# Kernel optimization log

Hardware: AMD Instinct MI355X
Metric: run time of the kernel (lower is better)

## Reference

```python
import jax, jax.numpy as jnp
import numpy as np

B_, S_, D_ = 2, 1024, 768
EXPAND, HEADDIM, DSTATE = 2, 64, 64
DINNER = EXPAND * D_            # 1536
NHEADS = DINNER // HEADDIM      # 24
DMLP = int(2.5 * D_)            # 1920
PROJ = 2 * DINNER + 2 * NHEADS * DSTATE + NHEADS + NHEADS * (DSTATE // 2)  # 6936


def rms_norm(x, w, eps=1e-5):
    return x * jax.lax.rsqrt(jnp.mean(x * x, axis=-1, keepdims=True) + eps) * w


def apply_rope(x, angles):
    # x: (..., d_state), angles: (..., d_state//2)
    x1 = x[..., 0::2]
    x2 = x[..., 1::2]
    c, s = jnp.cos(angles), jnp.sin(angles)
    even = c * x1 - s * x2
    odd = s * x1 + c * x2
    return jnp.stack([even, odd], axis=-1).reshape(x.shape)


def ssm_scan(x, A, Bm, Cm):
    # x: (b,s,h,p), A: (b,s,h), Bm/Cm: (b,s,h,n)
    b, s, h, p = x.shape
    n = Bm.shape[-1]

    def step(hstate, inp):
        x_t, A_t, B_t, C_t = inp
        hstate = hstate * jnp.exp(A_t)[:, :, None, None] + jnp.einsum('bhn,bhp->bhpn', B_t, x_t)
        y_t = jnp.einsum('bhpn,bhn->bhp', hstate, C_t)
        return hstate, y_t

    h0 = jnp.zeros((b, h, p, n), dtype=x.dtype)
    xs = (jnp.swapaxes(x, 0, 1), jnp.swapaxes(A, 0, 1),
          jnp.swapaxes(Bm, 0, 1), jnp.swapaxes(Cm, 0, 1))
    _, ys = jax.lax.scan(step, h0, xs)
    return jnp.swapaxes(ys, 0, 1)  # (b,s,h,p)


def setup_inputs() -> dict:
    key = jax.random.key(0)
    ks = jax.random.split(key, 16)
    sc = 0.02
    return {
        'x': jax.random.normal(ks[0], (B_, S_, D_), dtype=jnp.float32),
        'norm1_w': jnp.ones((D_,), jnp.float32),
        'norm2_w': jnp.ones((D_,), jnp.float32),
        'in_proj_w': jax.random.normal(ks[1], (PROJ, D_), jnp.float32) * sc,
        'out_proj_w': jax.random.normal(ks[2], (D_, DINNER), jnp.float32) * sc,
        'A_log': jax.random.uniform(ks[3], (NHEADS,), jnp.float32, -4.0, -1.0),
        'D': jnp.ones((NHEADS,), jnp.float32),
        'dt_bias': jax.random.uniform(ks[4], (NHEADS,), jnp.float32, 0.001, 0.1),
        'B_bias': jnp.ones((1, NHEADS, DSTATE), jnp.float32),
        'C_bias': jnp.ones((1, NHEADS, DSTATE), jnp.float32),
        'Bnorm_w': jnp.ones((DSTATE,), jnp.float32),
        'Cnorm_w': jnp.ones((DSTATE,), jnp.float32),
        'mlp_gate_w': jax.random.normal(ks[5], (DMLP, D_), jnp.float32) * sc,
        'mlp_up_w': jax.random.normal(ks[6], (DMLP, D_), jnp.float32) * sc,
        'mlp_down_w': jax.random.normal(ks[7], (D_, DMLP), jnp.float32) * sc,
    }


def reference(x, norm1_w, norm2_w, in_proj_w, out_proj_w, A_log, D, dt_bias,
              B_bias, C_bias, Bnorm_w, Cnorm_w, mlp_gate_w, mlp_up_w, mlp_down_w):
    b, s, _ = x.shape
    h = rms_norm(x, norm1_w)
    proj = jnp.einsum('bsd,od->bso', h, in_proj_w)
    i = 0
    z = proj[..., i:i + DINNER]; i += DINNER
    x_ssm = proj[..., i:i + DINNER]; i += DINNER
    Bm = proj[..., i:i + NHEADS * DSTATE].reshape(b, s, NHEADS, DSTATE); i += NHEADS * DSTATE
    Cm = proj[..., i:i + NHEADS * DSTATE].reshape(b, s, NHEADS, DSTATE); i += NHEADS * DSTATE
    dt = proj[..., i:i + NHEADS]; i += NHEADS
    theta = proj[..., i:].reshape(b, s, NHEADS, DSTATE // 2)

    dt = jax.nn.softplus(dt + dt_bias)                 # (b,s,h)
    A = -jnp.exp(A_log) * dt                           # (b,s,h)
    alpha = jnp.exp(A)
    gamma = (alpha - 1.0) / (A + 1e-6) * 0.5 + 1.0

    Bm = rms_norm(Bm, Bnorm_w) + B_bias
    Cm = rms_norm(Cm, Cnorm_w) + C_bias
    cum_theta = jnp.cumsum(dt[..., None] * theta, axis=1)
    Bm = apply_rope(Bm, cum_theta)
    Cm = apply_rope(Cm, cum_theta)

    x_ssm = x_ssm.reshape(b, s, NHEADS, HEADDIM)
    x_scaled = x_ssm * gamma[..., None]
    y = ssm_scan(x_scaled, A, Bm, Cm)                  # (b,s,h,p)
    skip = (D[None, None, :] * x_ssm.sum(-1))[..., None]  # (b,s,h,1)
    y = (y + skip).reshape(b, s, DINNER)
    y = y * (z * jax.nn.sigmoid(z))
    y = jnp.einsum('bsi,oi->bso', y, out_proj_w)
    x = x + y
    h2 = rms_norm(x, norm2_w)
    g = jnp.einsum('bsd,od->bso', h2, mlp_gate_w)
    u = jnp.einsum('bsd,od->bso', h2, mlp_up_w)
    mlp = jnp.einsum('bsi,oi->bso', (g * jax.nn.sigmoid(g)) * u, mlp_down_w)
    return x + mlp
```

## Files before the change

kernel.cpp:

```cpp
#include <hip/hip_runtime.h>

typedef unsigned short u16;
typedef __attribute__((ext_vector_type(8))) short short8;
typedef __attribute__((ext_vector_type(4))) float f32x4;

constexpr int B_N    = 2;
constexpr int SEQ    = 1024;
constexpr int DMODEL = 768;
constexpr int DINNER = 1536;
constexpr int NH     = 24;
constexpr int DMLP   = 1920;
constexpr int NPROJ  = 6936;
constexpr int PP     = 7040;
constexpr int MROWS  = B_N * SEQ;
constexpr int NCHUNK = 16;
constexpr int CLEN   = 64;

__device__ __forceinline__ u16 f2bf(float f) {
  union { float f; unsigned u; } x; x.f = f;
  unsigned r = x.u + 0x7fffu + ((x.u >> 16) & 1u);
  return (u16)(r >> 16);
}

__device__ __forceinline__ void gld_lds16(const u16* g, u16* l) {
  __builtin_amdgcn_global_load_lds((const __attribute__((address_space(1))) void*)g,
                                   (__attribute__((address_space(3))) void*)l, 16, 0, 0);
}

__device__ __forceinline__ short8 frag(const u16* base, int row, int cb) {
  return *(const short8*)(base + row * 64 + ((cb ^ (row & 7)) << 3));
}
__device__ __forceinline__ int swz_idx(int row, int e) {
  return (((e >> 3) ^ (row & 7)) << 3) | (e & 7);
}

constexpr size_t E0  = (size_t)PP * DMODEL;
constexpr size_t E0s = (size_t)NPROJ * DMODEL;
constexpr size_t E1  = (size_t)DMODEL * DINNER;
constexpr size_t E2  = (size_t)DMLP * DMODEL;
constexpr size_t ETOT = E0 + E1 + 3 * E2;

__global__ void cast_all_kernel(const float* __restrict__ w_in, const float* __restrict__ w_out,
                                const float* __restrict__ w_g, const float* __restrict__ w_u,
                                const float* __restrict__ w_d,
                                u16* __restrict__ wb_in, u16* __restrict__ wb_out,
                                u16* __restrict__ wb_gu, u16* __restrict__ wb_d) {
  size_t i = ((size_t)blockIdx.x * 256 + threadIdx.x) * 4;
  if (i >= ETOT) return;
  float4 v; u16* dst;
  if (i < E0) {
    dst = wb_in + i;
    if (i < E0s) v = *(const float4*)(w_in + i);
    else { v.x = v.y = v.z = v.w = 0.f; }
  } else if (i < E0 + E1) {
    size_t k = i - E0; dst = wb_out + k; v = *(const float4*)(w_out + k);
  } else if (i < E0 + E1 + E2) {
    size_t k = i - E0 - E1; dst = wb_gu + k; v = *(const float4*)(w_g + k);
  } else if (i < E0 + E1 + 2 * E2) {
    size_t k = i - E0 - E1 - E2; dst = wb_gu + E2 + k; v = *(const float4*)(w_u + k);
  } else {
    size_t k = i - E0 - E1 - 2 * E2; dst = wb_d + k; v = *(const float4*)(w_d + k);
  }
  short4 o;
  o.x = (short)f2bf(v.x); o.y = (short)f2bf(v.y);
  o.z = (short)f2bf(v.z); o.w = (short)f2bf(v.w);
  *(short4*)dst = o;
}

__global__ __launch_bounds__(256) void add_rmsnorm_kernel(
    const float* __restrict__ a, const float* __restrict__ b,
    const float* __restrict__ w, float* __restrict__ sum_out,
    u16* __restrict__ hout) {
  int row = blockIdx.x;
  int t = threadIdx.x;
  const float* pa = a + (size_t)row * DMODEL;
  const float* pb = b ? b + (size_t)row * DMODEL : nullptr;
  float v[3]; float ss = 0.f;
#pragma unroll
  for (int i = 0; i < 3; ++i) {
    int c = t + i * 256;
    float x = pa[c];
    if (pb) x += pb[c];
    v[i] = x; ss += x * x;
  }
#pragma unroll
  for (int o = 32; o > 0; o >>= 1) ss += __shfl_xor(ss, o);
  __shared__ float red[4];
  if ((t & 63) == 0) red[t >> 6] = ss;
  __syncthreads();
  ss = red[0] + red[1] + red[2] + red[3];
  float sc = rsqrtf(ss * (1.f / DMODEL) + 1e-5f);
#pragma unroll
  for (int i = 0; i < 3; ++i) {
    int c = t + i * 256;
    if (sum_out) sum_out[(size_t)row * DMODEL + c] = v[i];
    hout[(size_t)row * DMODEL + c] = f2bf(v[i] * sc * w[c]);
  }
}

template<int BM>
__global__ __launch_bounds__(256) void gemm_bt_kernel(
    const u16* __restrict__ A, const u16* __restrict__ Bw,
    float* __restrict__ C, int K, int ldc, const float* __restrict__ addsrc) {
  constexpr int MI = BM / 32;
  __shared__ u16 As[BM * 64];
  __shared__ u16 Bs[128 * 64];
  const int t = threadIdx.x;
  const int lane = t & 63;
  const int wave = t >> 6;
  const int wm = wave >> 1, wn = wave & 1;
  const int gx = gridDim.x, gy = gridDim.y;
  const int o = blockIdx.y * gx + blockIdx.x;
  const int nwg = gx * gy;
  const int cid = (o & 7) * (nwg >> 3) + (o >> 3);
  const int bx = cid / gy, by = cid - bx * gy;
  const int m0 = by * BM, n0 = bx * 128;
  f32x4 acc[MI][4] = {};
  const int rr = t >> 3;
  const int kc = (t & 7) * 8;
  const u16* ga = A + (size_t)(m0 + rr) * K + kc;
  const u16* gb = Bw + (size_t)(n0 + rr) * K + kc;
  for (int kt = 0; kt < K; kt += 64) {
    __syncthreads();
#pragma unroll
    for (int i = 0; i < MI; ++i)
      gld_lds16(ga + (size_t)i * 32 * K + kt, As + i * 2048 + t * 8);
#pragma unroll
    for (int i = 0; i < 4; ++i)
      gld_lds16(gb + (size_t)i * 32 * K + kt, Bs + i * 2048 + t * 8);
    __syncthreads();
#pragma unroll
    for (int kh = 0; kh < 2; ++kh) {
      short8 af[MI], bfr[4];
#pragma unroll
      for (int i = 0; i < MI; ++i)
        af[i] = *(const short8*)(As + (wm * (BM / 2) + i * 16 + (lane & 15)) * 64 + kh * 32 + (lane >> 4) * 8);
#pragma unroll
      for (int j = 0; j < 4; ++j)
        bfr[j] = *(const short8*)(Bs + (wn * 64 + j * 16 + (lane & 15)) * 64 + kh * 32 + (lane >> 4) * 8);
#pragma unroll
      for (int i = 0; i < MI; ++i)
#pragma unroll
        for (int j = 0; j < 4; ++j)
          acc[i][j] = __builtin_amdgcn_mfma_f32_16x16x32_bf16(af[i], bfr[j], acc[i][j], 0, 0, 0);
    }
  }
  const int cr = (lane >> 4) * 4;
  const int cc = lane & 15;
#pragma unroll
  for (int i = 0; i < MI; ++i) {
#pragma unroll
    for (int j = 0; j < 4; ++j) {
      int row = m0 + wm * (BM / 2) + i * 16 + cr;
      int col = n0 + wn * 64 + j * 16 + cc;
      float* cp = C + (size_t)row * ldc + col;
      if (addsrc) {
        const float* ap = addsrc + (size_t)row * ldc + col;
#pragma unroll
        for (int r = 0; r < 4; ++r) cp[(size_t)r * ldc] = acc[i][j][r] + ap[(size_t)r * ldc];
      } else {
#pragma unroll
        for (int r = 0; r < 4; ++r) cp[(size_t)r * ldc] = acc[i][j][r];
      }
    }
  }
}

__global__ __launch_bounds__(256) void prep_kernel(
    float* __restrict__ proj, const float* __restrict__ A_log,
    const float* __restrict__ Dv, const float* __restrict__ dt_bias,
    const float* __restrict__ B_bias, const float* __restrict__ C_bias,
    const float* __restrict__ Bnw, const float* __restrict__ Cnw,
    float* __restrict__ Abuf, float* __restrict__ skip_b,
    float* __restrict__ dtheta) {
  int wid = blockIdx.x * 4 + (threadIdx.x >> 6);
  int lane = threadIdx.x & 63;
  int m = wid / NH, h = wid - m * NH;
  float* row = proj + (size_t)m * PP;

  float Braw = row[3072 + h * 64 + lane];
  float Craw = row[4608 + h * 64 + lane];
  float sb = Braw * Braw, sc2 = Craw * Craw;
#pragma unroll
  for (int o = 32; o > 0; o >>= 1) { sb += __shfl_xor(sb, o); sc2 += __shfl_xor(sc2, o); }
  float rb = rsqrtf(sb * (1.f / 64.f) + 1e-5f);
  float rc = rsqrtf(sc2 * (1.f / 64.f) + 1e-5f);
  row[3072 + h * 64 + lane] = Braw * rb * Bnw[lane] + B_bias[h * 64 + lane];
  row[4608 + h * 64 + lane] = Craw * rc * Cnw[lane] + C_bias[h * 64 + lane];

  float dtr = row[6144 + h] + dt_bias[h];
  float dt = dtr > 20.f ? dtr : log1pf(expf(dtr));
  float A = -expf(A_log[h]) * dt;
  float alpha = expf(A);
  float gamma = (alpha - 1.f) / (A + 1e-6f) * 0.5f + 1.f;

  float xv = row[1536 + h * 64 + lane];
  float sx = xv;
#pragma unroll
  for (int o = 32; o > 0; o >>= 1) sx += __shfl_xor(sx, o);
  row[1536 + h * 64 + lane] = xv * gamma;

  if (lane == 0) {
    Abuf[(size_t)m * NH + h] = A;
    skip_b[(size_t)m * NH + h] = Dv[h] * sx;
  }
  if (lane < 32) {
    float th = row[6168 + h * 32 + lane];
    dtheta[(size_t)m * 768 + h * 32 + lane] = dt * th;
  }
}

__global__ __launch_bounds__(256) void cumsum_a_kernel(float* __restrict__ dtheta,
                                                       float* __restrict__ ctot) {
  int bid = blockIdx.x;
  int cb = bid % 3, rest = bid / 3;
  int c = rest & 15, b = rest >> 4;
  int col = cb * 256 + threadIdx.x;
  float* p = dtheta + ((size_t)(b * SEQ + c * CLEN)) * 768 + col;
  float acc = 0.f;
#pragma unroll 4
  for (int s = 0; s < CLEN; ++s) {
    acc += p[(size_t)s * 768];
    p[(size_t)s * 768] = acc;
  }
  ctot[((size_t)b * NCHUNK + c) * 768 + col] = acc;
}

__global__ void cumsum_b_kernel(float* __restrict__ ctot) {
  int tid = blockIdx.x * 256 + threadIdx.x;
  int b = tid / 768, col = tid - b * 768;
  float pre = 0.f;
#pragma unroll
  for (int c = 0; c < NCHUNK; ++c) {
    size_t o = ((size_t)b * NCHUNK + c) * 768 + col;
    float v = ctot[o];
    ctot[o] = pre;
    pre += v;
  }
}

__global__ __launch_bounds__(256) void houtA_kernel(
    const float* __restrict__ proj, const float* __restrict__ Abuf,
    const float* __restrict__ dtheta, const float* __restrict__ ctot,
    float* __restrict__ Lbuf, float* __restrict__ Hbuf) {
  int c = blockIdx.x & 15, bh = blockIdx.x >> 4;
  int b = bh / NH, h = bh - b * NH;
  int t = threadIdx.x, w = t >> 6, l = t & 63;
  __shared__ float sTmp[64][65];
  __shared__ u16 sBT[64 * 64];
  __shared__ u16 sXT[64 * 64];
  __shared__ float sRatio[64];
  int m0 = b * SEQ + c * CLEN;
  if (w == 0) {
    float v = Abuf[(size_t)(m0 + l) * NH + h];
#pragma unroll
    for (int o = 1; o < 64; o <<= 1) {
      float u = __shfl_up(v, o);
      if (l >= o) v += u;
    }
    Lbuf[(size_t)(m0 + l) * NH + h] = v;
    float L63 = __shfl(v, 63);
    sRatio[l] = expf(L63 - v);
  }
  int rr = t >> 2, q = t & 3;
  {
    const float* row = proj + (size_t)(m0 + rr) * PP + 3072 + h * 64;
    const float* ang = dtheta + (size_t)(m0 + rr) * 768 + h * 32;
    const float* angc = ctot + ((size_t)(b * NCHUNK + c)) * 768 + h * 32;
#pragma unroll
    for (int k = 0; k < 4; ++k) {
      int e = q * 16 + k * 4;
      float4 v = *(const float4*)(row + e);
      int j0 = e >> 1;
      float s0, c0, s1, c1;
      sincosf(ang[j0] + angc[j0], &s0, &c0);
      sincosf(ang[j0 + 1] + angc[j0 + 1], &s1, &c1);
      float4 ov;
      ov.x = c0 * v.x - s0 * v.y; ov.y = s0 * v.x + c0 * v.y;
      ov.z = c1 * v.z - s1 * v.w; ov.w = s1 * v.z + c1 * v.w;
      *(float4*)&sTmp[rr][e] = ov;
    }
  }
  __syncthreads();
  {
#pragma unroll
    for (int k = 0; k < 8; ++k) {
      int tw = (l + w * 8 + k) & 31;
      int t0 = tw * 2;
      unsigned pk = (unsigned)f2bf(sTmp[t0][l]) | ((unsigned)f2bf(sTmp[t0 + 1][l]) << 16);
      *(unsigned*)(sBT + l * 64 + swz_idx(l, t0)) = pk;
    }
  }
  __syncthreads();
  {
    const float* row = proj + (size_t)(m0 + rr) * PP + 1536 + h * 64;
#pragma unroll
    for (int k = 0; k < 4; ++k) {
      int e = q * 16 + k * 4;
      *(float4*)&sTmp[rr][e] = *(const float4*)(row + e);
    }
  }
  __syncthreads();
  {
#pragma unroll
    for (int k = 0; k < 8; ++k) {
      int tw = (l + w * 8 + k) & 31;
      int t0 = tw * 2;
      float v0 = sTmp[t0][l] * sRatio[t0];
      float v1 = sTmp[t0 + 1][l] * sRatio[t0 + 1];
      unsigned pk = (unsigned)f2bf(v0) | ((unsigned)f2bf(v1) << 16);
      *(unsigned*)(sXT + l * 64 + swz_idx(l, t0)) = pk;
    }
  }
  __syncthreads();
  f32x4 acc[4] = {};
#pragma unroll
  for (int kh = 0; kh < 2; ++kh) {
    int cb = kh * 4 + (l >> 4);
    short8 af = frag(sXT, w * 16 + (l & 15), cb);
#pragma unroll
    for (int j = 0; j < 4; ++j)
      acc[j] = __builtin_amdgcn_mfma_f32_16x16x32_bf16(af, frag(sBT, j * 16 + (l & 15), cb), acc[j], 0, 0, 0);
  }
  float* Hp = Hbuf + ((size_t)(bh * NCHUNK + c)) * 4096;
  int pr = w * 16 + ((l >> 4) << 2);
#pragma unroll
  for (int j = 0; j < 4; ++j)
#pragma unroll
    for (int r = 0; r < 4; ++r)
      Hp[(size_t)(pr + r) * 64 + j * 16 + (l & 15)] = acc[j][r];
}

__global__ __launch_bounds__(256) void scan2_kernel(
    float* __restrict__ Hbuf, const float* __restrict__ Lbuf) {
  int bh = blockIdx.x;
  int b = bh / NH, h = bh - b * NH;
  int e = threadIdx.x * 16;
  float S[16];
#pragma unroll
  for (int j = 0; j < 16; ++j) S[j] = 0.f;
  for (int c = 0; c < NCHUNK; ++c) {
    float* Hp = Hbuf + ((size_t)(bh * NCHUNK + c)) * 4096 + e;
    float P = expf(Lbuf[(size_t)(b * SEQ + c * CLEN + CLEN - 1) * NH + h]);
#pragma unroll
    for (int j = 0; j < 16; j += 4) {
      float4 loc = *(float4*)(Hp + j);
      float4 sv; sv.x = S[j]; sv.y = S[j + 1]; sv.z = S[j + 2]; sv.w = S[j + 3];
      *(float4*)(Hp + j) = sv;
      S[j]     = P * S[j]     + loc.x;
      S[j + 1] = P * S[j + 1] + loc.y;
      S[j + 2] = P * S[j + 2] + loc.z;
      S[j + 3] = P * S[j + 3] + loc.w;
    }
  }
}

__global__ __launch_bounds__(256) void intraB_kernel(
    const float* __restrict__ proj, const float* __restrict__ Hbuf,
    const float* __restrict__ Lbuf, const float* __restrict__ skip_b,
    const float* __restrict__ dtheta, const float* __restrict__ ctot,
    u16* __restrict__ actb) {
  int c = blockIdx.x & 15, bh = blockIdx.x >> 4;
  int b = bh / NH, h = bh - b * NH;
  int t = threadIdx.x, w = t >> 6, l = t & 63;
  __shared__ u16 sC[64 * 64];
  __shared__ u16 sBH[64 * 64];
  __shared__ u16 sXT[64 * 64];
  __shared__ union UU { float tmp[64][65]; u16 gm[64 * 64]; } uS;
  __shared__ float sL[64], sSkip[64];
  int m0 = b * SEQ + c * CLEN;
  if (w == 0) {
    sL[l] = Lbuf[(size_t)(m0 + l) * NH + h];
    sSkip[l] = skip_b[(size_t)(m0 + l) * NH + h];
  }
  int rr = t >> 2, q = t & 3;
  const float* ang = dtheta + (size_t)(m0 + rr) * 768 + h * 32;
  const float* angc = ctot + ((size_t)(b * NCHUNK + c)) * 768 + h * 32;
  {
    const float* rowC = proj + (size_t)(m0 + rr) * PP + 4608 + h * 64;
    const float* rowX = proj + (size_t)(m0 + rr) * PP + 1536 + h * 64;
#pragma unroll
    for (int k = 0; k < 4; ++k) {
      int e = q * 16 + k * 4;
      float4 v = *(const float4*)(rowC + e);
      int j0 = e >> 1;
      float s0, c0, s1, c1;
      sincosf(ang[j0] + angc[j0], &s0, &c0);
      sincosf(ang[j0 + 1] + angc[j0 + 1], &s1, &c1);
      unsigned lo = (unsigned)f2bf(c0 * v.x - s0 * v.y) | ((unsigned)f2bf(s0 * v.x + c0 * v.y) << 16);
      unsigned hi = (unsigned)f2bf(c1 * v.z - s1 * v.w) | ((unsigned)f2bf(s1 * v.z + c1 * v.w) << 16);
      int idx = swz_idx(rr, e);
      *(unsigned*)(sC + rr * 64 + idx) = lo;
      *(unsigned*)(sC + rr * 64 + idx + 2) = hi;
      *(float4*)&uS.tmp[rr][e] = *(const float4*)(rowX + e);
    }
  }
  __syncthreads();
  {
#pragma unroll
    for (int k = 0; k < 8; ++k) {
      int tw = (l + w * 8 + k) & 31;
      int t0 = tw * 2;
      unsigned pk = (unsigned)f2bf(uS.tmp[t0][l]) | ((unsigned)f2bf(uS.tmp[t0 + 1][l]) << 16);
      *(unsigned*)(sXT + l * 64 + swz_idx(l, t0)) = pk;
    }
    const float* rowB = proj + (size_t)(m0 + rr) * PP + 3072 + h * 64;
#pragma unroll
    for (int k = 0; k < 4; ++k) {
      int e = q * 16 + k * 4;
      float4 v = *(const float4*)(rowB + e);
      int j0 = e >> 1;
      float s0, c0, s1, c1;
      sincosf(ang[j0] + angc[j0], &s0, &c0);
      sincosf(ang[j0 + 1] + angc[j0 + 1], &s1, &c1);
      unsigned lo = (unsigned)f2bf(c0 * v.x - s0 * v.y) | ((unsigned)f2bf(s0 * v.x + c0 * v.y) << 16);
      unsigned hi = (unsigned)f2bf(c1 * v.z - s1 * v.w) | ((unsigned)f2bf(s1 * v.z + c1 * v.w) << 16);
      int idx = swz_idx(rr, e);
      *(unsigned*)(sBH + rr * 64 + idx) = lo;
      *(unsigned*)(sBH + rr * 64 + idx + 2) = hi;
    }
  }
  __syncthreads();
  f32x4 g4[4] = {};
#pragma unroll
  for (int kh = 0; kh < 2; ++kh) {
    int cb = kh * 4 + (l >> 4);
    short8 af = frag(sC, w * 16 + (l & 15), cb);
#pragma unroll
    for (int j = 0; j < 4; ++j)
      g4[j] = __builtin_amdgcn_mfma_f32_16x16x32_bf16(af, frag(sBH, j * 16 + (l & 15), cb), g4[j], 0, 0, 0);
  }
  __syncthreads();
  {
    int sr = w * 16 + ((l >> 4) << 2);
#pragma unroll
    for (int j = 0; j < 4; ++j) {
      int tc = j * 16 + (l & 15);
#pragma unroll
      for (int r = 0; r < 4; ++r) {
        int s = sr + r;
        float gv = (tc <= s) ? g4[j][r] * expf(sL[s] - sL[tc]) : 0.f;
        uS.gm[s * 64 + swz_idx(s, tc)] = f2bf(gv);
      }
    }
    const float* Hp = Hbuf + ((size_t)(bh * NCHUNK + c)) * 4096 + rr * 64;
#pragma unroll
    for (int k = 0; k < 4; ++k) {
      int e = q * 16 + k * 4;
      float4 v = *(const float4*)(Hp + e);
      unsigned lo = (unsigned)f2bf(v.x) | ((unsigned)f2bf(v.y) << 16);
      unsigned hi = (unsigned)f2bf(v.z) | ((unsigned)f2bf(v.w) << 16);
      int idx = swz_idx(rr, e);
      *(unsigned*)(sBH + rr * 64 + idx) = lo;
      *(unsigned*)(sBH + rr * 64 + idx + 2) = hi;
    }
  }
  __syncthreads();
  f32x4 y1[4] = {}, y2[4] = {};
#pragma unroll
  for (int kh = 0; kh < 2; ++kh) {
    int cb = kh * 4 + (l >> 4);
    short8 ag = frag(uS.gm, w * 16 + (l & 15), cb);
    short8 ac = frag(sC, w * 16 + (l & 15), cb);
#pragma unroll
    for (int j = 0; j < 4; ++j) {
      y1[j] = __builtin_amdgcn_mfma_f32_16x16x32_bf16(ag, frag(sXT, j * 16 + (l & 15), cb), y1[j], 0, 0, 0);
      y2[j] = __builtin_amdgcn_mfma_f32_16x16x32_bf16(ac, frag(sBH, j * 16 + (l & 15), cb), y2[j], 0, 0, 0);
    }
  }
  int sr = w * 16 + ((l >> 4) << 2);
#pragma unroll
  for (int r = 0; r < 4; ++r) {
    int s = sr + r;
    float scale = expf(sL[s]);
    float skp = sSkip[s];
    size_t mrow = (size_t)(m0 + s);
#pragma unroll
    for (int j = 0; j < 4; ++j) {
      int p = j * 16 + (l & 15);
      float y = y1[j][r] + scale * y2[j][r] + skp;
      float z = proj[mrow * PP + h * 64 + p];
      float sg = 1.f / (1.f + expf(-z));
      actb[mrow * DINNER + h * 64 + p] = f2bf(y * z * sg);
    }
  }
}

__global__ void glu_kernel(const float* __restrict__ gu_all, u16* __restrict__ gub) {
  int i = blockIdx.x * 256 + threadIdx.x;
  int m = i / DMLP;
  int ci = i - m * DMLP;
  float gv = gu_all[(size_t)m * 2 * DMLP + ci];
  float uv = gu_all[(size_t)m * 2 * DMLP + DMLP + ci];
  float s = gv / (1.f + expf(-gv));
  gub[i] = f2bf(s * uv);
}

extern "C" void kernel_launch(void* const* d_in, const int* in_sizes, int n_in,
                              void* d_out, int out_size, void* d_ws, size_t ws_size,
                              hipStream_t stream) {
  (void)in_sizes; (void)n_in; (void)out_size; (void)ws_size;
  const float* x      = (const float*)d_in[0];
  const float* n1w    = (const float*)d_in[1];
  const float* n2w    = (const float*)d_in[2];
  const float* w_in   = (const float*)d_in[3];
  const float* w_out  = (const float*)d_in[4];
  const float* A_log  = (const float*)d_in[5];
  const float* Dv     = (const float*)d_in[6];
  const float* dt_b   = (const float*)d_in[7];
  const float* B_bias = (const float*)d_in[8];
  const float* C_bias = (const float*)d_in[9];
  const float* Bnw    = (const float*)d_in[10];
  const float* Cnw    = (const float*)d_in[11];
  const float* w_g    = (const float*)d_in[12];
  const float* w_u    = (const float*)d_in[13];
  const float* w_d    = (const float*)d_in[14];
  float* out = (float*)d_out;

  char* ws = (char*)d_ws;
  size_t off = 0;
  auto alloc = [&](size_t bytes) -> char* {
    char* p = ws + off;
    off = (off + bytes + 255) & ~(size_t)255;
    return p;
  };
  u16*   wb_in  = (u16*)  alloc(E0 * 2);
  u16*   wb_out = (u16*)  alloc(E1 * 2);
  u16*   wb_gu  = (u16*)  alloc(E2 * 2 * 2);
  u16*   wb_d   = (u16*)  alloc(E2 * 2);
  u16*   h1     = (u16*)  alloc((size_t)MROWS * DMODEL * 2);
  float* proj   = (float*)alloc((size_t)MROWS * PP * 4);
  float* Abuf   = (float*)alloc((size_t)MROWS * NH * 4);
  float* skip_b = (float*)alloc((size_t)MROWS * NH * 4);
  float* Lbuf   = (float*)alloc((size_t)MROWS * NH * 4);
  float* dtheta = (float*)alloc((size_t)MROWS * 768 * 4);
  float* ctot   = (float*)alloc((size_t)B_N * NCHUNK * 768 * 4);
  float* Hbuf   = (float*)alloc((size_t)B_N * NH * NCHUNK * 4096 * 4);
  u16*   actb   = (u16*)  alloc((size_t)MROWS * DINNER * 2);
  float* tmp1   = (float*)alloc((size_t)MROWS * DMODEL * 4);
  float* x2     = (float*)alloc((size_t)MROWS * DMODEL * 4);
  u16*   h2     = (u16*)  alloc((size_t)MROWS * DMODEL * 2);
  float* gu_all = proj;
  u16*   gub    = (u16*)(proj + (size_t)MROWS * 2 * DMLP);
  float* mlpbuf = (float*)((char*)gub + (size_t)MROWS * DMLP * 2 + 256);
  (void)mlpbuf;

  cast_all_kernel<<<(int)((ETOT / 4 + 255) / 256), 256, 0, stream>>>(
      w_in, w_out, w_g, w_u, w_d, wb_in, wb_out, wb_gu, wb_d);
  add_rmsnorm_kernel<<<MROWS, 256, 0, stream>>>(x, nullptr, n1w, nullptr, h1);
  {
    dim3 g(PP / 128, MROWS / 128);
    gemm_bt_kernel<128><<<g, 256, 0, stream>>>(h1, wb_in, proj, DMODEL, PP, nullptr);
  }
  prep_kernel<<<MROWS * NH / 4, 256, 0, stream>>>(proj, A_log, Dv, dt_b, B_bias, C_bias,
                                                  Bnw, Cnw, Abuf, skip_b, dtheta);
  cumsum_a_kernel<<<B_N * NCHUNK * 3, 256, 0, stream>>>(dtheta, ctot);
  cumsum_b_kernel<<<6, 256, 0, stream>>>(ctot);
  houtA_kernel<<<B_N * NH * NCHUNK, 256, 0, stream>>>(proj, Abuf, dtheta, ctot, Lbuf, Hbuf);
  scan2_kernel<<<B_N * NH, 256, 0, stream>>>(Hbuf, Lbuf);
  intraB_kernel<<<B_N * NH * NCHUNK, 256, 0, stream>>>(proj, Hbuf, Lbuf, skip_b,
                                                       dtheta, ctot, actb);
  {
    dim3 g(DMODEL / 128, MROWS / 64);
    gemm_bt_kernel<64><<<g, 256, 0, stream>>>(actb, wb_out, tmp1, DINNER, DMODEL, nullptr);
  }
  add_rmsnorm_kernel<<<MROWS, 256, 0, stream>>>(x, tmp1, n2w, x2, h2);
  {
    dim3 g(2 * DMLP / 128, MROWS / 128);
    gemm_bt_kernel<128><<<g, 256, 0, stream>>>(h2, wb_gu, gu_all, DMODEL, 2 * DMLP, nullptr);
  }
  glu_kernel<<<MROWS * DMLP / 256, 256, 0, stream>>>(gu_all, gub);
  {
    dim3 g(DMODEL / 128, MROWS / 64);
    gemm_bt_kernel<64><<<g, 256, 0, stream>>>(gub, wb_d, out, DMLP, DMODEL, x2);
  }
}
```

Baseline: 341.2 us.

## Store projection output in bf16 and fuse SwiGLU into gate/up GEMM epilogue

```diff
diff --git a/kernel.cpp b/kernel.cpp
--- a/kernel.cpp
+++ b/kernel.cpp
@@ -20,6 +20,9 @@
   union { float f; unsigned u; } x; x.f = f;
   unsigned r = x.u + 0x7fffu + ((x.u >> 16) & 1u);
   return (u16)(r >> 16);
+}
+__device__ __forceinline__ float bf2f(u16 b) {
+  union { unsigned u; float f; } x; x.u = ((unsigned)b) << 16; return x.f;
 }
 
 __device__ __forceinline__ void gld_lds16(const u16* g, u16* l) {
@@ -54,10 +57,12 @@
     else { v.x = v.y = v.z = v.w = 0.f; }
   } else if (i < E0 + E1) {
     size_t k = i - E0; dst = wb_out + k; v = *(const float4*)(w_out + k);
-  } else if (i < E0 + E1 + E2) {
-    size_t k = i - E0 - E1; dst = wb_gu + k; v = *(const float4*)(w_g + k);
   } else if (i < E0 + E1 + 2 * E2) {
-    size_t k = i - E0 - E1 - E2; dst = wb_gu + E2 + k; v = *(const float4*)(w_u + k);
+    size_t k = i - E0 - E1;
+    size_t r = k / DMODEL, col = k - r * DMODEL;
+    const float* src = (r & 1) ? w_u : w_g;
+    v = *(const float4*)(src + (r >> 1) * DMODEL + col);
+    dst = wb_gu + k;
   } else {
     size_t k = i - E0 - E1 - 2 * E2; dst = wb_d + k; v = *(const float4*)(w_d + k);
   }
@@ -98,10 +103,10 @@
   }
 }
 
-template<int BM>
+template<int BM, int MODE>
 __global__ __launch_bounds__(256) void gemm_bt_kernel(
     const u16* __restrict__ A, const u16* __restrict__ Bw,
-    float* __restrict__ C, int K, int ldc, const float* __restrict__ addsrc) {
+    void* __restrict__ Cv, int K, int ldc, const float* __restrict__ addsrc) {
   constexpr int MI = BM / 32;
   __shared__ u16 As[BM * 64];
   __shared__ u16 Bs[128 * 64];
@@ -153,21 +158,41 @@
     for (int j = 0; j < 4; ++j) {
       int row = m0 + wm * (BM / 2) + i * 16 + cr;
       int col = n0 + wn * 64 + j * 16 + cc;
-      float* cp = C + (size_t)row * ldc + col;
-      if (addsrc) {
-        const float* ap = addsrc + (size_t)row * ldc + col;
-#pragma unroll
-        for (int r = 0; r < 4; ++r) cp[(size_t)r * ldc] = acc[i][j][r] + ap[(size_t)r * ldc];
+      if (MODE == 0) {
+        float* C = (float*)Cv;
+        float* cp = C + (size_t)row * ldc + col;
+        if (addsrc) {
+          const float* ap = addsrc + (size_t)row * ldc + col;
+#pragma unroll
+          for (int r = 0; r < 4; ++r) cp[(size_t)r * ldc] = acc[i][j][r] + ap[(size_t)r * ldc];
+        } else {
+#pragma unroll
+          for (int r = 0; r < 4; ++r) cp[(size_t)r * ldc] = acc[i][j][r];
+        }
+      } else if (MODE == 1) {
+        u16* C = (u16*)Cv;
+#pragma unroll
+        for (int r = 0; r < 4; ++r)
+          C[(size_t)(row + r) * ldc + col] = f2bf(acc[i][j][r]);
       } else {
-#pragma unroll
-        for (int r = 0; r < 4; ++r) cp[(size_t)r * ldc] = acc[i][j][r];
+        u16* C = (u16*)Cv;
+#pragma unroll
+        for (int r = 0; r < 4; ++r) {
+          float v = acc[i][j][r];
+          float p = __shfl_xor(v, 1);
+          if ((lane & 1) == 0) {
+            float g = v, u = p;
+            float res = g / (1.f + expf(-g)) * u;
+            C[(size_t)(row + r) * ldc + (col >> 1)] = f2bf(res);
+          }
+        }
       }
     }
   }
 }
 
 __global__ __launch_bounds__(256) void prep_kernel(
-    float* __restrict__ proj, const float* __restrict__ A_log,
+    u16* __restrict__ proj, const float* __restrict__ A_log,
     const float* __restrict__ Dv, const float* __restrict__ dt_bias,
     const float* __restrict__ B_bias, const float* __restrict__ C_bias,
     const float* __restrict__ Bnw, const float* __restrict__ Cnw,
@@ -176,36 +201,36 @@
   int wid = blockIdx.x * 4 + (threadIdx.x >> 6);
   int lane = threadIdx.x & 63;
   int m = wid / NH, h = wid - m * NH;
-  float* row = proj + (size_t)m * PP;
-
-  float Braw = row[3072 + h * 64 + lane];
-  float Craw = row[4608 + h * 64 + lane];
+  u16* row = proj + (size_t)m * PP;
+
+  float Braw = bf2f(row[3072 + h * 64 + lane]);
+  float Craw = bf2f(row[4608 + h * 64 + lane]);
   float sb = Braw * Braw, sc2 = Craw * Craw;
 #pragma unroll
   for (int o = 32; o > 0; o >>= 1) { sb += __shfl_xor(sb, o); sc2 += __shfl_xor(sc2, o); }
   float rb = rsqrtf(sb * (1.f / 64.f) + 1e-5f);
   float rc = rsqrtf(sc2 * (1.f / 64.f) + 1e-5f);
-  row[3072 + h * 64 + lane] = Braw * rb * Bnw[lane] + B_bias[h * 64 + lane];
-  row[4608 + h * 64 + lane] = Craw * rc * Cnw[lane] + C_bias[h * 64 + lane];
-
-  float dtr = row[6144 + h] + dt_bias[h];
+  row[3072 + h * 64 + lane] = f2bf(Braw * rb * Bnw[lane] + B_bias[h * 64 + lane]);
+  row[4608 + h * 64 + lane] = f2bf(Craw * rc * Cnw[lane] + C_bias[h * 64 + lane]);
+
+  float dtr = bf2f(row[6144 + h]) + dt_bias[h];
   float dt = dtr > 20.f ? dtr : log1pf(expf(dtr));
   float A = -expf(A_log[h]) * dt;
   float alpha = expf(A);
   float gamma = (alpha - 1.f) / (A + 1e-6f) * 0.5f + 1.f;
 
-  float xv = row[1536 + h * 64 + lane];
+  float xv = bf2f(row[1536 + h * 64 + lane]);
   float sx = xv;
 #pragma unroll
   for (int o = 32; o > 0; o >>= 1) sx += __shfl_xor(sx, o);
-  row[1536 + h * 64 + lane] = xv * gamma;
+  row[1536 + h * 64 + lane] = f2bf(xv * gamma);
 
   if (lane == 0) {
     Abuf[(size_t)m * NH + h] = A;
     skip_b[(size_t)m * NH + h] = Dv[h] * sx;
   }
   if (lane < 32) {
-    float th = row[6168 + h * 32 + lane];
+    float th = bf2f(row[6168 + h * 32 + lane]);
     dtheta[(size_t)m * 768 + h * 32 + lane] = dt * th;
   }
 }
@@ -240,7 +265,7 @@
 }
 
 __global__ __launch_bounds__(256) void houtA_kernel(
-    const float* __restrict__ proj, const float* __restrict__ Abuf,
+    const u16* __restrict__ proj, const float* __restrict__ Abuf,
     const float* __restrict__ dtheta, const float* __restrict__ ctot,
     float* __restrict__ Lbuf, float* __restrict__ Hbuf) {
   int c = blockIdx.x & 15, bh = blockIdx.x >> 4;
@@ -264,20 +289,22 @@
   }
   int rr = t >> 2, q = t & 3;
   {
-    const float* row = proj + (size_t)(m0 + rr) * PP + 3072 + h * 64;
+    const u16* row = proj + (size_t)(m0 + rr) * PP + 3072 + h * 64;
     const float* ang = dtheta + (size_t)(m0 + rr) * 768 + h * 32;
     const float* angc = ctot + ((size_t)(b * NCHUNK + c)) * 768 + h * 32;
 #pragma unroll
     for (int k = 0; k < 4; ++k) {
       int e = q * 16 + k * 4;
-      float4 v = *(const float4*)(row + e);
+      short4 sv = *(const short4*)(row + e);
       int j0 = e >> 1;
       float s0, c0, s1, c1;
       sincosf(ang[j0] + angc[j0], &s0, &c0);
       sincosf(ang[j0 + 1] + angc[j0 + 1], &s1, &c1);
+      float vx = bf2f((u16)sv.x), vy = bf2f((u16)sv.y);
+      float vz = bf2f((u16)sv.z), vw = bf2f((u16)sv.w);
       float4 ov;
-      ov.x = c0 * v.x - s0 * v.y; ov.y = s0 * v.x + c0 * v.y;
-      ov.z = c1 * v.z - s1 * v.w; ov.w = s1 * v.z + c1 * v.w;
+      ov.x = c0 * vx - s0 * vy; ov.y = s0 * vx + c0 * vy;
+      ov.z = c1 * vz - s1 * vw; ov.w = s1 * vz + c1 * vw;
       *(float4*)&sTmp[rr][e] = ov;
     }
   }
@@ -293,11 +320,15 @@
   }
   __syncthreads();
   {
-    const float* row = proj + (size_t)(m0 + rr) * PP + 1536 + h * 64;
+    const u16* row = proj + (size_t)(m0 + rr) * PP + 1536 + h * 64;
 #pragma unroll
     for (int k = 0; k < 4; ++k) {
       int e = q * 16 + k * 4;
-      *(float4*)&sTmp[rr][e] = *(const float4*)(row + e);
+      short4 sv = *(const short4*)(row + e);
+      float4 ov;
+      ov.x = bf2f((u16)sv.x); ov.y = bf2f((u16)sv.y);
+      ov.z = bf2f((u16)sv.z); ov.w = bf2f((u16)sv.w);
+      *(float4*)&sTmp[rr][e] = ov;
     }
   }
   __syncthreads();
@@ -356,7 +387,7 @@
 }
 
 __global__ __launch_bounds__(256) void intraB_kernel(
-    const float* __restrict__ proj, const float* __restrict__ Hbuf,
+    const u16* __restrict__ proj, const float* __restrict__ Hbuf,
     const float* __restrict__ Lbuf, const float* __restrict__ skip_b,
     const float* __restrict__ dtheta, const float* __restrict__ ctot,
     u16* __restrict__ actb) {
@@ -377,22 +408,28 @@
   const float* ang = dtheta + (size_t)(m0 + rr) * 768 + h * 32;
   const float* angc = ctot + ((size_t)(b * NCHUNK + c)) * 768 + h * 32;
   {
-    const float* rowC = proj + (size_t)(m0 + rr) * PP + 4608 + h * 64;
-    const float* rowX = proj + (size_t)(m0 + rr) * PP + 1536 + h * 64;
+    const u16* rowC = proj + (size_t)(m0 + rr) * PP + 4608 + h * 64;
+    const u16* rowX = proj + (size_t)(m0 + rr) * PP + 1536 + h * 64;
 #pragma unroll
     for (int k = 0; k < 4; ++k) {
       int e = q * 16 + k * 4;
-      float4 v = *(const float4*)(rowC + e);
+      short4 sv = *(const short4*)(rowC + e);
       int j0 = e >> 1;
       float s0, c0, s1, c1;
       sincosf(ang[j0] + angc[j0], &s0, &c0);
       sincosf(ang[j0 + 1] + angc[j0 + 1], &s1, &c1);
-      unsigned lo = (unsigned)f2bf(c0 * v.x - s0 * v.y) | ((unsigned)f2bf(s0 * v.x + c0 * v.y) << 16);
-      unsigned hi = (unsigned)f2bf(c1 * v.z - s1 * v.w) | ((unsigned)f2bf(s1 * v.z + c1 * v.w) << 16);
+      float vx = bf2f((u16)sv.x), vy = bf2f((u16)sv.y);
+      float vz = bf2f((u16)sv.z), vw = bf2f((u16)sv.w);
+      unsigned lo = (unsigned)f2bf(c0 * vx - s0 * vy) | ((unsigned)f2bf(s0 * vx + c0 * vy) << 16);
+      unsigned hi = (unsigned)f2bf(c1 * vz - s1 * vw) | ((unsigned)f2bf(s1 * vz + c1 * vw) << 16);
       int idx = swz_idx(rr, e);
       *(unsigned*)(sC + rr * 64 + idx) = lo;
       *(unsigned*)(sC + rr * 64 + idx + 2) = hi;
-      *(float4*)&uS.tmp[rr][e] = *(const float4*)(rowX + e);
+      short4 xv = *(const short4*)(rowX + e);
+      float4 ov;
+      ov.x = bf2f((u16)xv.x); ov.y = bf2f((u16)xv.y);
+      ov.z = bf2f((u16)xv.z); ov.w = bf2f((u16)xv.w);
+      *(float4*)&uS.tmp[rr][e] = ov;
     }
   }
   __syncthreads();
@@ -404,17 +441,19 @@
       unsigned pk = (unsigned)f2bf(uS.tmp[t0][l]) | ((unsigned)f2bf(uS.tmp[t0 + 1][l]) << 16);
       *(unsigned*)(sXT + l * 64 + swz_idx(l, t0)) = pk;
     }
-    const float* rowB = proj + (size_t)(m0 + rr) * PP + 3072 + h * 64;
+    const u16* rowB = proj + (size_t)(m0 + rr) * PP + 3072 + h * 64;
 #pragma unroll
     for (int k = 0; k < 4; ++k) {
       int e = q * 16 + k * 4;
-      float4 v = *(const float4*)(rowB + e);
+      short4 sv = *(const short4*)(rowB + e);
       int j0 = e >> 1;
       float s0, c0, s1, c1;
       sincosf(ang[j0] + angc[j0], &s0, &c0);
       sincosf(ang[j0 + 1] + angc[j0 + 1], &s1, &c1);
-      unsigned lo = (unsigned)f2bf(c0 * v.x - s0 * v.y) | ((unsigned)f2bf(s0 * v.x + c0 * v.y) << 16);
-      unsigned hi = (unsigned)f2bf(c1 * v.z - s1 * v.w) | ((unsigned)f2bf(s1 * v.z + c1 * v.w) << 16);
+      float vx = bf2f((u16)sv.x), vy = bf2f((u16)sv.y);
+      float vz = bf2f((u16)sv.z), vw = bf2f((u16)sv.w);
+      unsigned lo = (unsigned)f2bf(c0 * vx - s0 * vy) | ((unsigned)f2bf(s0 * vx + c0 * vy) << 16);
+      unsigned hi = (unsigned)f2bf(c1 * vz - s1 * vw) | ((unsigned)f2bf(s1 * vz + c1 * vw) << 16);
       int idx = swz_idx(rr, e);
       *(unsigned*)(sBH + rr * 64 + idx) = lo;
       *(unsigned*)(sBH + rr * 64 + idx + 2) = hi;
@@ -479,21 +518,11 @@
     for (int j = 0; j < 4; ++j) {
       int p = j * 16 + (l & 15);
       float y = y1[j][r] + scale * y2[j][r] + skp;
-      float z = proj[mrow * PP + h * 64 + p];
+      float z = bf2f(proj[mrow * PP + h * 64 + p]);
       float sg = 1.f / (1.f + expf(-z));
       actb[mrow * DINNER + h * 64 + p] = f2bf(y * z * sg);
     }
   }
-}
-
-__global__ void glu_kernel(const float* __restrict__ gu_all, u16* __restrict__ gub) {
-  int i = blockIdx.x * 256 + threadIdx.x;
-  int m = i / DMLP;
-  int ci = i - m * DMLP;
-  float gv = gu_all[(size_t)m * 2 * DMLP + ci];
-  float uv = gu_all[(size_t)m * 2 * DMLP + DMLP + ci];
-  float s = gv / (1.f + expf(-gv));
-  gub[i] = f2bf(s * uv);
 }
 
 extern "C" void kernel_launch(void* const* d_in, const int* in_sizes, int n_in,
@@ -529,7 +558,7 @@
   u16*   wb_gu  = (u16*)  alloc(E2 * 2 * 2);
   u16*   wb_d   = (u16*)  alloc(E2 * 2);
   u16*   h1     = (u16*)  alloc((size_t)MROWS * DMODEL * 2);
-  float* proj   = (float*)alloc((size_t)MROWS * PP * 4);
+  u16*   proj   = (u16*)  alloc((size_t)MROWS * PP * 2);
   float* Abuf   = (float*)alloc((size_t)MROWS * NH * 4);
   float* skip_b = (float*)alloc((size_t)MROWS * NH * 4);
   float* Lbuf   = (float*)alloc((size_t)MROWS * NH * 4);
@@ -540,17 +569,14 @@
   float* tmp1   = (float*)alloc((size_t)MROWS * DMODEL * 4);
   float* x2     = (float*)alloc((size_t)MROWS * DMODEL * 4);
   u16*   h2     = (u16*)  alloc((size_t)MROWS * DMODEL * 2);
-  float* gu_all = proj;
-  u16*   gub    = (u16*)(proj + (size_t)MROWS * 2 * DMLP);
-  float* mlpbuf = (float*)((char*)gub + (size_t)MROWS * DMLP * 2 + 256);
-  (void)mlpbuf;
+  u16*   gub    = (u16*)  alloc((size_t)MROWS * DMLP * 2);
 
   cast_all_kernel<<<(int)((ETOT / 4 + 255) / 256), 256, 0, stream>>>(
       w_in, w_out, w_g, w_u, w_d, wb_in, wb_out, wb_gu, wb_d);
   add_rmsnorm_kernel<<<MROWS, 256, 0, stream>>>(x, nullptr, n1w, nullptr, h1);
   {
     dim3 g(PP / 128, MROWS / 128);
-    gemm_bt_kernel<128><<<g, 256, 0, stream>>>(h1, wb_in, proj, DMODEL, PP, nullptr);
+    gemm_bt_kernel<128, 1><<<g, 256, 0, stream>>>(h1, wb_in, proj, DMODEL, PP, nullptr);
   }
   prep_kernel<<<MROWS * NH / 4, 256, 0, stream>>>(proj, A_log, Dv, dt_b, B_bias, C_bias,
                                                   Bnw, Cnw, Abuf, skip_b, dtheta);
@@ -562,16 +588,15 @@
                                                        dtheta, ctot, actb);
   {
     dim3 g(DMODEL / 128, MROWS / 64);
-    gemm_bt_kernel<64><<<g, 256, 0, stream>>>(actb, wb_out, tmp1, DINNER, DMODEL, nullptr);
+    gemm_bt_kernel<64, 0><<<g, 256, 0, stream>>>(actb, wb_out, tmp1, DINNER, DMODEL, nullptr);
   }
   add_rmsnorm_kernel<<<MROWS, 256, 0, stream>>>(x, tmp1, n2w, x2, h2);
   {
     dim3 g(2 * DMLP / 128, MROWS / 128);
-    gemm_bt_kernel<128><<<g, 256, 0, stream>>>(h2, wb_gu, gu_all, DMODEL, 2 * DMLP, nullptr);
-  }
-  glu_kernel<<<MROWS * DMLP / 256, 256, 0, stream>>>(gu_all, gub);
+    gemm_bt_kernel<128, 2><<<g, 256, 0, stream>>>(h2, wb_gu, gub, DMODEL, DMLP, nullptr);
+  }
   {
     dim3 g(DMODEL / 128, MROWS / 64);
-    gemm_bt_kernel<64><<<g, 256, 0, stream>>>(gub, wb_d, out, DMLP, DMODEL, x2);
-  }
-}
+    gemm_bt_kernel<64, 0><<<g, 256, 0, stream>>>(gub, wb_d, out, DMLP, DMODEL, x2);
+  }
+}
```

Result: faster. 333.5 us (-2.3%).
